# Kernel tuning notes

Measured on AMD Instinct MI355X. Metric: run time of the kernel, lower is better.

Reference implementation:

```python
import jax, jax.numpy as jnp
import numpy as np

D_MODEL = 4096
N_TYPES = 6  # fixed event_types list in the module


def setup_inputs() -> dict:
    key = jax.random.key(0)
    ks = jax.random.split(key, 7)
    E, B, d = 131072, 16384, D_MODEL
    return {
        "event_type": jax.random.randint(ks[0], (E,), 0, N_TYPES),
        "confidence": jax.random.uniform(ks[1], (E,), jnp.float32),
        "location": jax.random.uniform(ks[2], (E, 2), jnp.float32) * jnp.array([640.0, 480.0], jnp.float32),
        "batch_idx": jax.random.randint(ks[3], (E,), 0, B),
        "batch_size": B,
        "type_emb": jax.random.normal(ks[4], (N_TYPES, d // 4), jnp.float32),
        "W1": jax.random.normal(ks[5], (d // 2, d // 4 + 3), jnp.float32) / np.sqrt(d // 4 + 3).astype(np.float32),
        "b1": jnp.zeros((d // 2,), jnp.float32),
        "W2": jax.random.normal(ks[6], (d, d // 2), jnp.float32) / np.sqrt(d // 2).astype(np.float32),
        "b2": jnp.zeros((d,), jnp.float32),
    }


def reference(event_type, confidence, location, batch_idx, batch_size, type_emb, W1, b1, W2, b2):
    E = confidence.shape[0]
    B = batch_size
    # per-batch-slot max confidence (empty slots -> -inf)
    seg_max = jax.ops.segment_max(confidence, batch_idx, num_segments=B)
    is_top = confidence == seg_max[batch_idx]
    # first event attaining the max (matches torch's max-over-list semantics)
    cand = jnp.where(is_top, jnp.arange(E), E)
    top_idx = jnp.full((B,), E, dtype=cand.dtype).at[batch_idx].min(cand)
    has_event = top_idx < E
    safe_idx = jnp.where(has_event, top_idx, 0)

    emb = type_emb[event_type[safe_idx]]                 # [B, d/4]
    c = confidence[safe_idx][:, None]                    # [B, 1]
    loc = location[safe_idx] / jnp.array([640.0, 480.0], jnp.float32)  # [B, 2]
    feats = jnp.concatenate([emb, c, loc], axis=-1)      # [B, d/4 + 3]

    h = jax.nn.relu(feats @ W1.T + b1)                   # [B, d/2]
    out = h @ W2.T + b2                                  # [B, d]
    return jnp.where(has_event[:, None], out, jnp.zeros((), out.dtype))
```

## Files before the change

kernel.cpp:

```cpp
#include <hip/hip_runtime.h>
#include <hip/hip_bf16.h>

#define NT 6
#define BM 256
#define BN 256
#define BK 32
#define SLOT 16384

typedef __attribute__((ext_vector_type(4))) float f32x4;
typedef __attribute__((ext_vector_type(8))) short bf16x8;

__device__ __forceinline__ short f2bf(float f) {
    __hip_bfloat16 h = __float2bfloat16(f);
    return (short)__builtin_bit_cast(unsigned short, h);
}

__global__ void k_segmax(const float* __restrict__ conf,
                         const int* __restrict__ bidx,
                         unsigned long long* __restrict__ packed, int E) {
    int i = blockIdx.x * blockDim.x + threadIdx.x;
    if (i >= E) return;
    unsigned cb = __float_as_uint(conf[i]);
    unsigned long long p = ((unsigned long long)cb << 32) | (unsigned)(~(unsigned)i);
    atomicMax(&packed[bidx[i]], p);
}

__global__ void k_base(const float* __restrict__ emb, const float* __restrict__ W1,
                       const float* __restrict__ b1, float* __restrict__ base,
                       float* __restrict__ vecs, int d2, int d4) {
    int gw = (blockIdx.x * blockDim.x + threadIdx.x) >> 6;
    int lane = threadIdx.x & 63;
    int t = gw / d2, n = gw % d2;
    const float* e = emb + (size_t)t * d4;
    const float* w = W1 + (size_t)n * (d4 + 3);
    float s = 0.f;
    for (int k = lane; k < d4; k += 64) s += e[k] * w[k];
#pragma unroll
    for (int m = 32; m; m >>= 1) s += __shfl_xor(s, m);
    if (lane == 0) {
        base[gw] = s + b1[n];
        if (t == 0) {
            vecs[n]          = w[d4];
            vecs[d2 + n]     = w[d4 + 1];
            vecs[2 * d2 + n] = w[d4 + 2];
        }
    }
}

__global__ void k_w2cast(const float* __restrict__ W2, short* __restrict__ W2b, long n) {
    long i = ((long)blockIdx.x * blockDim.x + threadIdx.x) * 8;
    if (i >= n) return;
    bf16x8 v;
#pragma unroll
    for (int j = 0; j < 8; ++j) v[j] = f2bf(W2[i + j]);
    *(bf16x8*)(W2b + i) = v;
}

__global__ void k_h(const unsigned long long* __restrict__ packed,
                    const int* __restrict__ etype, const float* __restrict__ loc,
                    const float* __restrict__ base, const float* __restrict__ vecs,
                    float* __restrict__ mask, short* __restrict__ h, int d2) {
    int b = blockIdx.x;
    int tid = threadIdx.x;
    unsigned long long p = packed[b];
    bool has = (p != 0ULL);
    float conf = 0.f, lx = 0.f, ly = 0.f;
    int t = 0;
    if (has) {
        unsigned idx = ~(unsigned)(p & 0xFFFFFFFFu);
        conf = __uint_as_float((unsigned)(p >> 32));
        t  = etype[idx];
        lx = loc[2 * (size_t)idx]     * (1.0f / 640.0f);
        ly = loc[2 * (size_t)idx + 1] * (1.0f / 480.0f);
    }
    if (tid == 0) mask[b] = has ? 1.0f : 0.0f;
    const float* bs = base + (size_t)t * d2;
    const float* cv = vecs;
    const float* xv = vecs + d2;
    const float* yv = vecs + 2 * d2;
    int n0 = tid * 8;
    bf16x8 v;
#pragma unroll
    for (int j = 0; j < 8; ++j) {
        int n = n0 + j;
        float g = bs[n] + conf * cv[n] + lx * xv[n] + ly * yv[n];
        g = fmaxf(g, 0.f);
        v[j] = has ? f2bf(g) : (short)0;
    }
    *(bf16x8*)(h + (size_t)b * d2 + n0) = v;
}


#define GLL(src, dst) __builtin_amdgcn_global_load_lds(                      \
    (const __attribute__((address_space(1))) void*)(src),                    \
    (__attribute__((address_space(3))) void*)(dst), 16, 0, 0)

#define STAGE4(slotp) do {                                                   \
    GLL(pa0, (slotp) + dA0); GLL(pa1, (slotp) + dA1);                        \
    GLL(pb0, (slotp) + dB0); GLL(pb1, (slotp) + dB1);                        \
    pa0 += BK; pa1 += BK; pb0 += BK; pb1 += BK; } while (0)

#define COMPUTE(slotp) do {                                                  \
    const short* sa_ = (slotp) + aoff;                                       \
    const short* sb_ = (slotp) + boff;                                       \
    bf16x8 af[8], bv[4];                                                     \
    _Pragma("unroll") for (int m = 0; m < 8; ++m)                            \
        af[m] = *(const bf16x8*)(sa_ + m * 512);                             \
    _Pragma("unroll") for (int n = 0; n < 4; ++n)                            \
        bv[n] = *(const bf16x8*)(sb_ + n * 512);                             \
    __builtin_amdgcn_s_setprio(1);                                           \
    _Pragma("unroll") for (int m = 0; m < 8; ++m)                            \
        _Pragma("unroll") for (int n = 0; n < 4; ++n)                        \
            acc[m][n] = __builtin_amdgcn_mfma_f32_16x16x32_bf16(             \
                af[m], bv[n], acc[m][n], 0, 0, 0);                           \
    __builtin_amdgcn_s_setprio(0);                                           \
} while (0)

#define PHASE_END(VMN) do {                                                  \
    __builtin_amdgcn_sched_barrier(0);                                       \
    asm volatile("s_waitcnt vmcnt(" VMN ")" ::: "memory");                   \
    asm volatile("s_barrier" ::: "memory");                                  \
    __builtin_amdgcn_sched_barrier(0); } while (0)

__global__ __launch_bounds__(512, 2)
void k_gemm(const short* __restrict__ A, const short* __restrict__ Bm,
            const float* __restrict__ b2, const float* __restrict__ mask,
            float* __restrict__ C, int M, int N, int K, int nbn) {
    __shared__ __align__(16) short lds[4 * SLOT];

    int tid = threadIdx.x;
    int lane = tid & 63;
    int wave = tid >> 6;
    int wr = wave >> 2, wc = wave & 3;

    int bid = blockIdx.x;
    int wg = (bid & 7) * ((int)gridDim.x >> 3) + (bid >> 3);
    int bm = wg / nbn, bn = wg % nbn;
    int row0 = bm * BM, col0 = bn * BN;

    int srow = tid >> 2;
    int chunkL = (tid & 3) ^ (srow & 3);
    const short* pa0 = A + (size_t)(row0 + srow) * K + chunkL * 8;
    const short* pa1 = pa0 + (size_t)128 * K;
    const short* pb0 = Bm + (size_t)(col0 + srow) * K + chunkL * 8;
    const short* pb1 = pb0 + (size_t)128 * K;
    int dA0 = tid * 8, dA1 = 4096 + tid * 8;
    int dB0 = 8192 + tid * 8, dB1 = 12288 + tid * 8;

    int frow = lane & 15, fk = lane >> 4;
    int cp = fk ^ (frow & 3);
    int aoff = (wr * 128 + frow) * 32 + cp * 8;
    int boff = 8192 + (wc * 64 + frow) * 32 + cp * 8;

    f32x4 acc[8][4] = {};

    int KT = K / BK;

    STAGE4(lds + 0 * SLOT);
    STAGE4(lds + 1 * SLOT);
    STAGE4(lds + 2 * SLOT);
    PHASE_END("8");

#pragma unroll 1
    for (int t = 0; t < KT - 3; ++t) {
        short* slotw = lds + ((t + 3) & 3) * SLOT;
        const short* slotr = lds + (t & 3) * SLOT;
        STAGE4(slotw);
        COMPUTE(slotr);
        PHASE_END("8");
    }
    COMPUTE(lds + ((KT - 3) & 3) * SLOT);
    PHASE_END("4");
    COMPUTE(lds + ((KT - 2) & 3) * SLOT);
    PHASE_END("0");
    COMPUTE(lds + ((KT - 1) & 3) * SLOT);

#pragma unroll
    for (int m = 0; m < 8; ++m) {
        int rbase = row0 + wr * 128 + m * 16 + (lane >> 4) * 4;
#pragma unroll
        for (int j = 0; j < 4; ++j) {
            int r = rbase + j;
            float mk = mask[r];
#pragma unroll
            for (int n = 0; n < 4; ++n) {
                int c = col0 + wc * 64 + n * 16 + frow;
                C[(size_t)r * N + c] = (acc[m][n][j] + b2[c]) * mk;
            }
        }
    }
}

extern "C" void kernel_launch(void* const* d_in, const int* in_sizes, int n_in,
                              void* d_out, int out_size, void* d_ws, size_t ws_size,
                              hipStream_t stream) {
    const int* etype   = (const int*)d_in[0];
    const float* conf  = (const float*)d_in[1];
    const float* loc   = (const float*)d_in[2];
    const int* bidx    = (const int*)d_in[3];
    const float* emb   = (const float*)d_in[5];
    const float* W1    = (const float*)d_in[6];
    const float* b1    = (const float*)d_in[7];
    const float* W2    = (const float*)d_in[8];
    const float* b2    = (const float*)d_in[9];
    float* out = (float*)d_out;

    int E  = in_sizes[0];
    int d2 = in_sizes[7];
    int d  = in_sizes[9];
    int d4 = in_sizes[5] / NT;
    int B  = out_size / d;

    char* ws = (char*)d_ws;
    unsigned long long* packed = (unsigned long long*)ws;
    float* mask = (float*)(ws + (size_t)B * 8);
    float* base = mask + B;
    float* vecs = base + NT * d2;
    short* w2b  = (short*)(vecs + 3 * d2);
    short* h    = w2b + (size_t)d * d2;

    hipMemsetAsync(packed, 0, (size_t)B * 8, stream);
    k_segmax<<<(E + 255) / 256, 256, 0, stream>>>(conf, bidx, packed, E);
    k_base<<<(NT * d2) / 4, 256, 0, stream>>>(emb, W1, b1, base, vecs, d2, d4);
    long nw2 = (long)d * d2;
    k_w2cast<<<(int)(nw2 / 8 / 256), 256, 0, stream>>>(W2, w2b, nw2);
    k_h<<<B, 256, 0, stream>>>(packed, etype, loc, base, vecs, mask, h, d2);
    int nbm = B / BM, nbn = d / BN;
    k_gemm<<<dim3(nbm * nbn), dim3(512), 0, stream>>>(h, w2b, b2, mask, out, B, d, d2, nbn);
}
```

Measured before the change: 329.1 us.

## Split GEMM K-step into two half-phases interleaving LDS reads, loads and MFMAs

Each K iteration of the bf16 GEMM now runs as two sub-phases: read B plus half of A from LDS, issue the A global-to-LDS loads, then run the MFMAs for the first four M tiles; then read the other half of A, issue the B loads, and run the second four M tiles. The goal is to overlap LDS reads and global load issue with MFMA work, and to cut register pressure by holding only four A fragments at a time. The LDS XOR swizzle also changes to use (row>>1)&3, aiming to reduce bank conflicts. The cost is extra barriers per iteration and a rewritten tail loop whose vmcnt accounting must stay correct.

```diff
diff --git a/kernel.cpp b/kernel.cpp
--- a/kernel.cpp
+++ b/kernel.cpp
@@ -100,27 +100,30 @@
     GLL(pb0, (slotp) + dB0); GLL(pb1, (slotp) + dB1);                        \
     pa0 += BK; pa1 += BK; pb0 += BK; pb1 += BK; } while (0)
 
-#define COMPUTE(slotp) do {                                                  \
-    const short* sa_ = (slotp) + aoff;                                       \
-    const short* sb_ = (slotp) + boff;                                       \
-    bf16x8 af[8], bv[4];                                                     \
-    _Pragma("unroll") for (int m = 0; m < 8; ++m)                            \
-        af[m] = *(const bf16x8*)(sa_ + m * 512);                             \
+#define READS_SP0(slotr) do {                                                \
+    const short* sa_ = (slotr) + aoff;                                       \
+    const short* sb_ = (slotr) + boff;                                       \
     _Pragma("unroll") for (int n = 0; n < 4; ++n)                            \
         bv[n] = *(const bf16x8*)(sb_ + n * 512);                             \
+    _Pragma("unroll") for (int m = 0; m < 4; ++m)                            \
+        af[m] = *(const bf16x8*)(sa_ + m * 512); } while (0)
+
+#define READS_SP1(slotr) do {                                                \
+    const short* sa_ = (slotr) + aoff + 2048;                                \
+    _Pragma("unroll") for (int m = 0; m < 4; ++m)                            \
+        af[m] = *(const bf16x8*)(sa_ + m * 512); } while (0)
+
+#define MFMA_HALF(mb) do {                                                   \
     __builtin_amdgcn_s_setprio(1);                                           \
-    _Pragma("unroll") for (int m = 0; m < 8; ++m)                            \
+    _Pragma("unroll") for (int m = 0; m < 4; ++m)                            \
         _Pragma("unroll") for (int n = 0; n < 4; ++n)                        \
-            acc[m][n] = __builtin_amdgcn_mfma_f32_16x16x32_bf16(             \
-                af[m], bv[n], acc[m][n], 0, 0, 0);                           \
-    __builtin_amdgcn_s_setprio(0);                                           \
-} while (0)
-
-#define PHASE_END(VMN) do {                                                  \
-    __builtin_amdgcn_sched_barrier(0);                                       \
-    asm volatile("s_waitcnt vmcnt(" VMN ")" ::: "memory");                   \
-    asm volatile("s_barrier" ::: "memory");                                  \
-    __builtin_amdgcn_sched_barrier(0); } while (0)
+            acc[(mb) + m][n] = __builtin_amdgcn_mfma_f32_16x16x32_bf16(      \
+                af[m], bv[n], acc[(mb) + m][n], 0, 0, 0);                    \
+    __builtin_amdgcn_s_setprio(0); } while (0)
+
+#define SBAR __builtin_amdgcn_sched_barrier(0)
+#define BARRIER __builtin_amdgcn_s_barrier()
+#define WAIT_LGKM0 asm volatile("s_waitcnt lgkmcnt(0)" ::: "memory")
 
 __global__ __launch_bounds__(512, 2)
 void k_gemm(const short* __restrict__ A, const short* __restrict__ Bm,
@@ -139,7 +142,7 @@
     int row0 = bm * BM, col0 = bn * BN;
 
     int srow = tid >> 2;
-    int chunkL = (tid & 3) ^ (srow & 3);
+    int chunkL = (tid & 3) ^ ((srow >> 1) & 3);
     const short* pa0 = A + (size_t)(row0 + srow) * K + chunkL * 8;
     const short* pa1 = pa0 + (size_t)128 * K;
     const short* pb0 = Bm + (size_t)(col0 + srow) * K + chunkL * 8;
@@ -148,32 +151,58 @@
     int dB0 = 8192 + tid * 8, dB1 = 12288 + tid * 8;
 
     int frow = lane & 15, fk = lane >> 4;
-    int cp = fk ^ (frow & 3);
+    int cp = fk ^ ((frow >> 1) & 3);
     int aoff = (wr * 128 + frow) * 32 + cp * 8;
     int boff = 8192 + (wc * 64 + frow) * 32 + cp * 8;
 
     f32x4 acc[8][4] = {};
+    bf16x8 af[4], bv[4];
 
     int KT = K / BK;
 
     STAGE4(lds + 0 * SLOT);
     STAGE4(lds + 1 * SLOT);
     STAGE4(lds + 2 * SLOT);
-    PHASE_END("8");
+    SBAR;
+    asm volatile("s_waitcnt vmcnt(8)" ::: "memory");
+    BARRIER;
 
 #pragma unroll 1
     for (int t = 0; t < KT - 3; ++t) {
+        const short* slotr = lds + (t & 3) * SLOT;
         short* slotw = lds + ((t + 3) & 3) * SLOT;
+        READS_SP0(slotr);
+        GLL(pa0, slotw + dA0); GLL(pa1, slotw + dA1);
+        SBAR; BARRIER; WAIT_LGKM0; SBAR;
+        MFMA_HALF(0);
+        SBAR; BARRIER;
+        READS_SP1(slotr);
+        GLL(pb0, slotw + dB0); GLL(pb1, slotw + dB1);
+        pa0 += BK; pa1 += BK; pb0 += BK; pb1 += BK;
+        SBAR; BARRIER; WAIT_LGKM0; SBAR;
+        MFMA_HALF(4);
+        SBAR;
+        asm volatile("s_waitcnt vmcnt(8)" ::: "memory");
+        BARRIER;
+    }
+
+#pragma unroll 1
+    for (int t = KT - 3; t < KT; ++t) {
         const short* slotr = lds + (t & 3) * SLOT;
-        STAGE4(slotw);
-        COMPUTE(slotr);
-        PHASE_END("8");
-    }
-    COMPUTE(lds + ((KT - 3) & 3) * SLOT);
-    PHASE_END("4");
-    COMPUTE(lds + ((KT - 2) & 3) * SLOT);
-    PHASE_END("0");
-    COMPUTE(lds + ((KT - 1) & 3) * SLOT);
+        READS_SP0(slotr);
+        SBAR; BARRIER; WAIT_LGKM0; SBAR;
+        MFMA_HALF(0);
+        SBAR; BARRIER;
+        READS_SP1(slotr);
+        SBAR; WAIT_LGKM0; SBAR;
+        MFMA_HALF(4);
+        if (t < KT - 1) {
+            SBAR;
+            if (t == KT - 3) asm volatile("s_waitcnt vmcnt(4)" ::: "memory");
+            else             asm volatile("s_waitcnt vmcnt(0)" ::: "memory");
+            BARRIER;
+        }
+    }
 
 #pragma unroll
     for (int m = 0; m < 8; ++m) {
```

Result: faster. 313.9 us (-4.6%).

## Restructure GEMM K-loop to sync every two tiles and change LDS swizzle

Applied to the files above, without the earlier changes.

The bf16 GEMM main loop now processes two K-tiles per iteration and does a single full vmcnt wait plus barrier per pair, where it used to sync after every tile. Prefetch depth drops from three tiles ahead to two. Global-to-LDS loads for a future tile are issued after the current tile's fragments are read from LDS. The LDS XOR swizzle now uses (row>>1)&3, meant to cut bank conflicts for the fragment reads. The intent is to halve barrier overhead, with the risk that the shallower prefetch and the full vmcnt(0) wait expose more global-memory latency.

```diff
diff --git a/kernel.cpp b/kernel.cpp
--- a/kernel.cpp
+++ b/kernel.cpp
@@ -100,27 +100,30 @@
     GLL(pb0, (slotp) + dB0); GLL(pb1, (slotp) + dB1);                        \
     pa0 += BK; pa1 += BK; pb0 += BK; pb1 += BK; } while (0)
 
-#define COMPUTE(slotp) do {                                                  \
-    const short* sa_ = (slotp) + aoff;                                       \
-    const short* sb_ = (slotp) + boff;                                       \
-    bf16x8 af[8], bv[4];                                                     \
-    _Pragma("unroll") for (int m = 0; m < 8; ++m)                            \
-        af[m] = *(const bf16x8*)(sa_ + m * 512);                             \
+#define SB __builtin_amdgcn_sched_barrier(0)
+
+#define TILE(T) do {                                                         \
+    const short* sr_ = lds + ((T) & 3) * SLOT;                               \
+    bf16x8 bv[4], a03[4], a47[4];                                            \
     _Pragma("unroll") for (int n = 0; n < 4; ++n)                            \
-        bv[n] = *(const bf16x8*)(sb_ + n * 512);                             \
+        bv[n] = *(const bf16x8*)(sr_ + boff + n * 512);                      \
+    _Pragma("unroll") for (int m = 0; m < 4; ++m)                            \
+        a03[m] = *(const bf16x8*)(sr_ + aoff + m * 512);                     \
+    _Pragma("unroll") for (int m = 0; m < 4; ++m)                            \
+        a47[m] = *(const bf16x8*)(sr_ + aoff + 2048 + m * 512);              \
+    if ((T) + 2 < KT) { short* sw_ = lds + (((T) + 2) & 3) * SLOT;           \
+                        STAGE4(sw_); }                                       \
     __builtin_amdgcn_s_setprio(1);                                           \
-    _Pragma("unroll") for (int m = 0; m < 8; ++m)                            \
-        _Pragma("unroll") for (int n = 0; n < 4; ++n)                        \
-            acc[m][n] = __builtin_amdgcn_mfma_f32_16x16x32_bf16(             \
-                af[m], bv[n], acc[m][n], 0, 0, 0);                           \
+    _Pragma("unroll") for (int m = 0; m < 4; ++m)                            \
+    _Pragma("unroll") for (int n = 0; n < 4; ++n)                            \
+        acc[m][n] = __builtin_amdgcn_mfma_f32_16x16x32_bf16(                 \
+            a03[m], bv[n], acc[m][n], 0, 0, 0);                              \
+    _Pragma("unroll") for (int m = 0; m < 4; ++m)                            \
+    _Pragma("unroll") for (int n = 0; n < 4; ++n)                            \
+        acc[4 + m][n] = __builtin_amdgcn_mfma_f32_16x16x32_bf16(             \
+            a47[m], bv[n], acc[4 + m][n], 0, 0, 0);                          \
     __builtin_amdgcn_s_setprio(0);                                           \
 } while (0)
-
-#define PHASE_END(VMN) do {                                                  \
-    __builtin_amdgcn_sched_barrier(0);                                       \
-    asm volatile("s_waitcnt vmcnt(" VMN ")" ::: "memory");                   \
-    asm volatile("s_barrier" ::: "memory");                                  \
-    __builtin_amdgcn_sched_barrier(0); } while (0)
 
 __global__ __launch_bounds__(512, 2)
 void k_gemm(const short* __restrict__ A, const short* __restrict__ Bm,
@@ -139,7 +142,7 @@
     int row0 = bm * BM, col0 = bn * BN;
 
     int srow = tid >> 2;
-    int chunkL = (tid & 3) ^ (srow & 3);
+    int chunkL = (tid & 3) ^ ((srow >> 1) & 3);
     const short* pa0 = A + (size_t)(row0 + srow) * K + chunkL * 8;
     const short* pa1 = pa0 + (size_t)128 * K;
     const short* pb0 = Bm + (size_t)(col0 + srow) * K + chunkL * 8;
@@ -148,7 +151,7 @@
     int dB0 = 8192 + tid * 8, dB1 = 12288 + tid * 8;
 
     int frow = lane & 15, fk = lane >> 4;
-    int cp = fk ^ (frow & 3);
+    int cp = fk ^ ((frow >> 1) & 3);
     int aoff = (wr * 128 + frow) * 32 + cp * 8;
     int boff = 8192 + (wc * 64 + frow) * 32 + cp * 8;
 
@@ -158,22 +161,21 @@
 
     STAGE4(lds + 0 * SLOT);
     STAGE4(lds + 1 * SLOT);
-    STAGE4(lds + 2 * SLOT);
-    PHASE_END("8");
+    asm volatile("s_waitcnt vmcnt(0)" ::: "memory");
+    __builtin_amdgcn_s_barrier();
+    SB;
 
 #pragma unroll 1
-    for (int t = 0; t < KT - 3; ++t) {
-        short* slotw = lds + ((t + 3) & 3) * SLOT;
-        const short* slotr = lds + (t & 3) * SLOT;
-        STAGE4(slotw);
-        COMPUTE(slotr);
-        PHASE_END("8");
-    }
-    COMPUTE(lds + ((KT - 3) & 3) * SLOT);
-    PHASE_END("4");
-    COMPUTE(lds + ((KT - 2) & 3) * SLOT);
-    PHASE_END("0");
-    COMPUTE(lds + ((KT - 1) & 3) * SLOT);
+    for (int t = 0; t < KT; t += 2) {
+        TILE(t);
+        TILE(t + 1);
+        SB;
+        if (t + 2 < KT) {
+            asm volatile("s_waitcnt vmcnt(0)" ::: "memory");
+            __builtin_amdgcn_s_barrier();
+            SB;
+        }
+    }
 
 #pragma unroll
     for (int m = 0; m < 8; ++m) {
```

Measured after the change: 307.8 us. 6.5% less time.
